# Performance work log

Hardware: AMD Instinct MI355X
Metric: run time of the kernel (lower is better)

The kernel has to match this reference:

```python
import jax, jax.numpy as jnp
import numpy as np

BASE_THETA = 0.5
K_DOP = 0.2
K_NOR = 0.15
K_SERO = 0.1
DIM = 1024


def setup_inputs() -> dict:
    key = jax.random.key(0)
    ks = jax.random.split(key, 9)
    scale = 1.0 / np.sqrt(DIM)
    x = jax.random.normal(ks[0], (2, 2048, DIM), dtype=jnp.float32)
    Wq = jax.random.normal(ks[1], (DIM, DIM), dtype=jnp.float32) * scale
    bq = jnp.zeros((DIM,), dtype=jnp.float32)
    Wk = jax.random.normal(ks[2], (DIM, DIM), dtype=jnp.float32) * scale
    bk = jnp.zeros((DIM,), dtype=jnp.float32)
    Wv = jax.random.normal(ks[3], (DIM, DIM), dtype=jnp.float32) * scale
    bv = jnp.zeros((DIM,), dtype=jnp.float32)
    Wo = jax.random.normal(ks[4], (DIM, DIM), dtype=jnp.float32) * scale
    bo = jnp.zeros((DIM,), dtype=jnp.float32)
    return {"x": x, "Wq": Wq, "bq": bq, "Wk": Wk, "bk": bk,
            "Wv": Wv, "bv": bv, "Wo": Wo, "bo": bo}


def reference(x, Wq, bq, Wk, bk, Wv, bv, Wo, bo):
    # Projections: torch nn.Linear computes x @ W.T + b
    q = jnp.einsum('bsd,ed->bse', x, Wq) + bq
    k = jnp.einsum('bsd,ed->bse', x, Wk) + bk
    v = jnp.einsum('bsd,ed->bse', x, Wv) + bv
    # Full [B, S, S] scores (no 1/sqrt(d) scaling in the original)
    qk = jnp.einsum('bsd,btd->bst', q, k)
    theta = (BASE_THETA
             + K_DOP * jax.nn.sigmoid(qk)
             + K_NOR * jnp.tanh(qk)
             + K_SERO * jax.nn.relu(qk))
    attn = jax.nn.softmax(theta, axis=-1)
    out = jnp.einsum('bst,btd->bsd', attn, v)
    return jnp.einsum('bsd,ed->bse', out, Wo) + bo
```

## Files before the change

kernel.cpp:

```cpp
#include <hip/hip_runtime.h>
#include <hip/hip_fp16.h>
#include <stdint.h>

typedef _Float16 f16;
typedef __attribute__((ext_vector_type(8))) _Float16 f16x8;
typedef __attribute__((ext_vector_type(4))) _Float16 f16x4;
typedef __attribute__((ext_vector_type(4))) float f32x4;

#define SEQ 2048
#define DIM 1024
#define NBATCH 2
#define MTOT 4096

__global__ void fill_kernel(float* p, float v, int n){
  int i = blockIdx.x * 256 + threadIdx.x;
  if (i < n) p[i] = v;
}

__global__ void cvt_all(const float* __restrict__ x, const float* __restrict__ Wq,
                        const float* __restrict__ Wk, const float* __restrict__ Wv,
                        const float* __restrict__ Wo,
                        f16* __restrict__ x16, f16* __restrict__ Wcat, f16* __restrict__ Wo16){
  int b = blockIdx.x;
  const float* src; f16* dst; int i;
  if (b < 4096){
    src = x; dst = x16; i = b * 256 + threadIdx.x;
  } else {
    int t = (b - 4096) >> 10;
    i = ((b - 4096) & 1023) * 256 + threadIdx.x;
    src = t == 0 ? Wq : t == 1 ? Wk : t == 2 ? Wv : Wo;
    dst = (t == 3) ? Wo16 : Wcat + (size_t)t * DIM * DIM;
  }
  float4 v = ((const float4*)src)[i];
  ((f16x4*)dst)[i] = (f16x4){(f16)v.x, (f16)v.y, (f16)v.z, (f16)v.w};
}

#define GLOAD16(SRC, DST) __builtin_amdgcn_global_load_lds( \
    (__attribute__((address_space(1))) void*)(SRC), \
    (__attribute__((address_space(3))) void*)(DST), 16, 0, 0)

__device__ __forceinline__ float theta_exp(float v){
  const float e1 = __expf(-v);
  const float sg = 1.f / (1.f + e1);
  const float e2 = e1 * e1;
  const float th = 2.f / (1.f + e2) - 1.f;
  const float theta = 0.5f + 0.2f * sg + 0.15f * th + 0.1f * fmaxf(v, 0.f);
  return __expf(fminf(theta - 10.f, 11.f));
}

__global__ __launch_bounds__(256, 3)
void gemm_qkv(const f16* __restrict__ A0, const f16* __restrict__ B0,
              f16* __restrict__ O0, f16* __restrict__ O1,
              const float* __restrict__ c0, const float* __restrict__ c1,
              const float* __restrict__ c2)
{
  __shared__ __align__(16) f16 As[8192];
  __shared__ __align__(16) f16 Bs[8192];
  const int tid  = threadIdx.x;
  const int lane = tid & 63;
  const int wid  = tid >> 6;
  const int bm = blockIdx.x, bn = blockIdx.y;

  const int s_r  = tid >> 3;
  const int s_cb = (tid & 7) ^ (s_r & 7);
  const f16* Ab = A0 + (long)(bm * 128 + s_r) * DIM + s_cb * 8;
  const f16* Bb = B0 + (long)(bn * 128 + s_r) * DIM + s_cb * 8;

  const int l15 = lane & 15, l7 = lane & 7, lhi = lane >> 4;
  const int wrow = (wid >> 1) * 64;
  const int wcol = (wid & 1) * 64;
  const int ar = (wrow + l15) * 64;
  const int br = (wcol + l15) * 64;
  const int cb0 = ((0 + lhi) ^ l7) * 8;
  const int cb1 = ((4 + lhi) ^ l7) * 8;

  f32x4 acc[4][4] = {};

#pragma unroll
  for (int t = 0; t < 16; ++t){
    __syncthreads();
    GLOAD16(Ab + (long)t*64,                  &As[       tid*8]);
    GLOAD16(Ab + (long)t*64 + (long)32 * DIM, &As[2048 + tid*8]);
    GLOAD16(Ab + (long)t*64 + (long)64 * DIM, &As[4096 + tid*8]);
    GLOAD16(Ab + (long)t*64 + (long)96 * DIM, &As[6144 + tid*8]);
    GLOAD16(Bb + (long)t*64,                  &Bs[       tid*8]);
    GLOAD16(Bb + (long)t*64 + (long)32 * DIM, &Bs[2048 + tid*8]);
    GLOAD16(Bb + (long)t*64 + (long)64 * DIM, &Bs[4096 + tid*8]);
    GLOAD16(Bb + (long)t*64 + (long)96 * DIM, &Bs[6144 + tid*8]);
    __syncthreads();
    f16x8 af[4], bf[4];
#pragma unroll
    for (int i = 0; i < 4; i++) af[i] = *(const f16x8*)&As[ar + i * 1024 + cb0];
#pragma unroll
    for (int j = 0; j < 4; j++) bf[j] = *(const f16x8*)&Bs[br + j * 1024 + cb0];
#pragma unroll
    for (int i = 0; i < 4; i++)
#pragma unroll
      for (int j = 0; j < 4; j++)
        acc[i][j] = __builtin_amdgcn_mfma_f32_16x16x32_f16(af[i], bf[j], acc[i][j], 0, 0, 0);
#pragma unroll
    for (int i = 0; i < 4; i++) af[i] = *(const f16x8*)&As[ar + i * 1024 + cb1];
#pragma unroll
    for (int j = 0; j < 4; j++) bf[j] = *(const f16x8*)&Bs[br + j * 1024 + cb1];
#pragma unroll
    for (int i = 0; i < 4; i++)
#pragma unroll
      for (int j = 0; j < 4; j++)
        acc[i][j] = __builtin_amdgcn_mfma_f32_16x16x32_f16(af[i], bf[j], acc[i][j], 0, 0, 0);
  }

  const int cc = l15;
  const int rr = lhi * 4;
#pragma unroll
  for (int i = 0; i < 4; i++)
#pragma unroll
    for (int j = 0; j < 4; j++){
      const int col = bn * 128 + wcol + j * 16 + cc;
      if (col < 2048){
        const float badd = (col < 1024) ? c0[col] : c1[col - 1024];
#pragma unroll
        for (int r = 0; r < 4; r++){
          const int row = bm * 128 + wrow + i * 16 + rr + r;
          O0[(long)row * 2048 + col] = (f16)(acc[i][j][r] + badd);
        }
      } else {
        const int dcol = col - 2048;
        const float badd = c2[dcol];
#pragma unroll
        for (int r = 0; r < 4; r++){
          const int row = bm * 128 + wrow + i * 16 + rr + r;
          O1[(long)row * DIM + dcol] = (f16)(acc[i][j][r] + badd);
        }
      }
    }
}

__global__ __launch_bounds__(256, 3)
void gemm_merged(const f16* __restrict__ qkcat, const f16* __restrict__ vbuf,
                 const f16* __restrict__ Wo16,
                 f16* __restrict__ Pbuf, f16* __restrict__ vWoT)
{
  __shared__ __align__(16) f16 As[8192];
  __shared__ __align__(16) f16 Bs[8192];
  const int tid  = threadIdx.x;
  const int lane = tid & 63;
  const int wid  = tid >> 6;
  const int l15 = lane & 15, l7 = lane & 7, lhi = lane >> 4;
  const int s_r  = tid >> 3;
  const int s_cb = (tid & 7) ^ (s_r & 7);
  const int cb0 = ((0 + lhi) ^ l7) * 8;
  const int cb1 = ((4 + lhi) ^ l7) * 8;
  const int cc = l15, rr = lhi * 4;
  const int wrow = (wid >> 1) * 64;
  const int wcol = (wid & 1) * 64;
  const int ar = (wrow + l15) * 64;
  const int br = (wcol + l15) * 64;
  const int r = blockIdx.x;

  if (r < 512){
    const int x = r & 7, i5 = r >> 3;
    const int bz = x >> 2;
    const int bn = (x & 3) * 4 + (i5 & 3);
    const int bm = i5 >> 2;
    const f16* Ab = qkcat + (long)bz * SEQ * 2048 + (long)(bm * 128 + s_r) * 2048 + s_cb * 8;
    const f16* Bb = qkcat + DIM + (long)bz * SEQ * 2048 + (long)(bn * 128 + s_r) * 2048 + s_cb * 8;

    f32x4 acc[4][4] = {};

#pragma unroll
    for (int t = 0; t < 16; ++t){
      __syncthreads();
      GLOAD16(Ab + (long)t*64,                   &As[       tid*8]);
      GLOAD16(Ab + (long)t*64 + (long)32 * 2048, &As[2048 + tid*8]);
      GLOAD16(Ab + (long)t*64 + (long)64 * 2048, &As[4096 + tid*8]);
      GLOAD16(Ab + (long)t*64 + (long)96 * 2048, &As[6144 + tid*8]);
      GLOAD16(Bb + (long)t*64,                   &Bs[       tid*8]);
      GLOAD16(Bb + (long)t*64 + (long)32 * 2048, &Bs[2048 + tid*8]);
      GLOAD16(Bb + (long)t*64 + (long)64 * 2048, &Bs[4096 + tid*8]);
      GLOAD16(Bb + (long)t*64 + (long)96 * 2048, &Bs[6144 + tid*8]);
      __syncthreads();
      f16x8 af[4], bf[4];
#pragma unroll
      for (int i = 0; i < 4; i++) af[i] = *(const f16x8*)&As[ar + i * 1024 + cb0];
#pragma unroll
      for (int j = 0; j < 4; j++) bf[j] = *(const f16x8*)&Bs[br + j * 1024 + cb0];
#pragma unroll
      for (int i = 0; i < 4; i++)
#pragma unroll
        for (int j = 0; j < 4; j++)
          acc[i][j] = __builtin_amdgcn_mfma_f32_16x16x32_f16(af[i], bf[j], acc[i][j], 0, 0, 0);
#pragma unroll
      for (int i = 0; i < 4; i++) af[i] = *(const f16x8*)&As[ar + i * 1024 + cb1];
#pragma unroll
      for (int j = 0; j < 4; j++) bf[j] = *(const f16x8*)&Bs[br + j * 1024 + cb1];
#pragma unroll
      for (int i = 0; i < 4; i++)
#pragma unroll
        for (int j = 0; j < 4; j++)
          acc[i][j] = __builtin_amdgcn_mfma_f32_16x16x32_f16(af[i], bf[j], acc[i][j], 0, 0, 0);
    }

#pragma unroll
    for (int i = 0; i < 4; i++)
#pragma unroll
      for (int rq = 0; rq < 4; rq++){
        const int row = bm * 128 + wrow + i * 16 + rr + rq;
#pragma unroll
        for (int j = 0; j < 4; j++){
          const int col = bn * 128 + wcol + j * 16 + cc;
          Pbuf[(long)bz * SEQ * SEQ + (long)row * SEQ + col] = (f16)theta_exp(acc[i][j][rq]);
        }
      }
  } else {
    const int rr2 = r - 512;
    const int x = rr2 & 7, i5 = rr2 >> 3;
    const int bz = x >> 2;
    const int bn = (x & 3) * 2 + (i5 & 1);
    const int bm = i5 >> 1;
    const f16* Ab = vbuf + (long)bz * SEQ * DIM + (long)(bm * 128 + s_r) * DIM + s_cb * 8;
    const f16* Bb = Wo16 + (long)(bn * 128 + s_r) * DIM + s_cb * 8;

    f32x4 acc[4][4] = {};

#pragma unroll
    for (int t = 0; t < 16; ++t){
      __syncthreads();
      GLOAD16(Ab + (long)t*64,                  &As[       tid*8]);
      GLOAD16(Ab + (long)t*64 + (long)32 * DIM, &As[2048 + tid*8]);
      GLOAD16(Ab + (long)t*64 + (long)64 * DIM, &As[4096 + tid*8]);
      GLOAD16(Ab + (long)t*64 + (long)96 * DIM, &As[6144 + tid*8]);
      GLOAD16(Bb + (long)t*64,                  &Bs[       tid*8]);
      GLOAD16(Bb + (long)t*64 + (long)32 * DIM, &Bs[2048 + tid*8]);
      GLOAD16(Bb + (long)t*64 + (long)64 * DIM, &Bs[4096 + tid*8]);
      GLOAD16(Bb + (long)t*64 + (long)96 * DIM, &Bs[6144 + tid*8]);
      __syncthreads();
      f16x8 af[4], bf[4];
#pragma unroll
      for (int i = 0; i < 4; i++) af[i] = *(const f16x8*)&As[ar + i * 1024 + cb0];
#pragma unroll
      for (int j = 0; j < 4; j++) bf[j] = *(const f16x8*)&Bs[br + j * 1024 + cb0];
#pragma unroll
      for (int i = 0; i < 4; i++)
#pragma unroll
        for (int j = 0; j < 4; j++)
          acc[i][j] = __builtin_amdgcn_mfma_f32_16x16x32_f16(af[i], bf[j], acc[i][j], 0, 0, 0);
#pragma unroll
      for (int i = 0; i < 4; i++) af[i] = *(const f16x8*)&As[ar + i * 1024 + cb1];
#pragma unroll
      for (int j = 0; j < 4; j++) bf[j] = *(const f16x8*)&Bs[br + j * 1024 + cb1];
#pragma unroll
      for (int i = 0; i < 4; i++)
#pragma unroll
        for (int j = 0; j < 4; j++)
          acc[i][j] = __builtin_amdgcn_mfma_f32_16x16x32_f16(af[i], bf[j], acc[i][j], 0, 0, 0);
    }

#pragma unroll
    for (int i = 0; i < 4; i++)
#pragma unroll
      for (int j = 0; j < 4; j++){
        const int col = bn * 128 + wcol + j * 16 + cc;
        const int row0 = bm * 128 + wrow + i * 16 + rr;
        f16x4 pk = {(f16)acc[i][j][0], (f16)acc[i][j][1],
                    (f16)acc[i][j][2], (f16)acc[i][j][3]};
        *(f16x4*)&vWoT[(long)bz * DIM * SEQ + (long)col * SEQ + row0] = pk;
      }
  }
}

__global__ __launch_bounds__(256, 4)
void gemm_final(const f16* __restrict__ Pb, const f16* __restrict__ Vw,
                float* __restrict__ psum, float* __restrict__ rowsum)
{
  __shared__ __align__(16) f16 As[8192];
  __shared__ __align__(16) f16 Bs[8192];
  const int tid  = threadIdx.x;
  const int lane = tid & 63;
  const int wid  = tid >> 6;
  const int bm = blockIdx.x, bn = blockIdx.y;
  const int bz = blockIdx.z >> 1, kh = blockIdx.z & 1;

  const f16* Ag = Pb + (long)bz * SEQ * SEQ + (long)kh * 1024;
  const f16* Bg = Vw + (long)bz * DIM * SEQ + (long)kh * 1024;

  const int s_r  = tid >> 3;
  const int s_cb = (tid & 7) ^ (s_r & 7);
  const f16* Ab = Ag + (long)(bm * 128 + s_r) * 2048 + s_cb * 8;
  const f16* Bb = Bg + (long)(bn * 128 + s_r) * 2048 + s_cb * 8;

  const int l15 = lane & 15, l7 = lane & 7, lhi = lane >> 4;
  const int wrow = (wid >> 1) * 64;
  const int wcol = (wid & 1) * 64;
  const int ar = (wrow + l15) * 64;
  const int br = (wcol + l15) * 64;
  const int cb0 = ((0 + lhi) ^ l7) * 8;
  const int cb1 = ((4 + lhi) ^ l7) * 8;
  const bool do_rs = ((wid & 1) == 0);

  f32x4 acc[4][4] = {};
  float rsum[4] = {0.f, 0.f, 0.f, 0.f};

#pragma unroll
  for (int t = 0; t < 16; ++t){
    __syncthreads();
    GLOAD16(Ab + (long)t*64,                   &As[       tid*8]);
    GLOAD16(Ab + (long)t*64 + (long)32 * 2048, &As[2048 + tid*8]);
    GLOAD16(Ab + (long)t*64 + (long)64 * 2048, &As[4096 + tid*8]);
    GLOAD16(Ab + (long)t*64 + (long)96 * 2048, &As[6144 + tid*8]);
    GLOAD16(Bb + (long)t*64,                   &Bs[       tid*8]);
    GLOAD16(Bb + (long)t*64 + (long)32 * 2048, &Bs[2048 + tid*8]);
    GLOAD16(Bb + (long)t*64 + (long)64 * 2048, &Bs[4096 + tid*8]);
    GLOAD16(Bb + (long)t*64 + (long)96 * 2048, &Bs[6144 + tid*8]);
    __syncthreads();
    f16x8 af[4], bf[4];
#pragma unroll
    for (int i = 0; i < 4; i++) af[i] = *(const f16x8*)&As[ar + i * 1024 + cb0];
#pragma unroll
    for (int j = 0; j < 4; j++) bf[j] = *(const f16x8*)&Bs[br + j * 1024 + cb0];
#pragma unroll
    for (int i = 0; i < 4; i++)
#pragma unroll
      for (int j = 0; j < 4; j++)
        acc[i][j] = __builtin_amdgcn_mfma_f32_16x16x32_f16(af[i], bf[j], acc[i][j], 0, 0, 0);
    if (do_rs){
#pragma unroll
      for (int i = 0; i < 4; i++)
#pragma unroll
        for (int e = 0; e < 8; e++) rsum[i] += (float)af[i][e];
    }
#pragma unroll
    for (int i = 0; i < 4; i++) af[i] = *(const f16x8*)&As[ar + i * 1024 + cb1];
#pragma unroll
    for (int j = 0; j < 4; j++) bf[j] = *(const f16x8*)&Bs[br + j * 1024 + cb1];
#pragma unroll
    for (int i = 0; i < 4; i++)
#pragma unroll
      for (int j = 0; j < 4; j++)
        acc[i][j] = __builtin_amdgcn_mfma_f32_16x16x32_f16(af[i], bf[j], acc[i][j], 0, 0, 0);
    if (do_rs){
#pragma unroll
      for (int i = 0; i < 4; i++)
#pragma unroll
        for (int e = 0; e < 8; e++) rsum[i] += (float)af[i][e];
    }
  }

  if (do_rs){
#pragma unroll
    for (int i = 0; i < 4; i++){
      rsum[i] += __shfl_xor(rsum[i], 16, 64);
      rsum[i] += __shfl_xor(rsum[i], 32, 64);
    }
    if (bn == 0 && lane < 16){
#pragma unroll
      for (int i = 0; i < 4; i++)
        rowsum[(long)kh * MTOT + bz * SEQ + bm * 128 + wrow + i * 16 + lane] = rsum[i];
    }
  }

  const int cc = l15;
  const int rr = lhi * 4;
  float* Po = psum + (long)kh * MTOT * DIM + (long)bz * SEQ * DIM;
#pragma unroll
  for (int i = 0; i < 4; i++)
#pragma unroll
    for (int j = 0; j < 4; j++){
      const int col = bn * 128 + wcol + j * 16 + cc;
#pragma unroll
      for (int r = 0; r < 4; r++){
        const int row = bm * 128 + wrow + i * 16 + rr + r;
        Po[(long)row * DIM + col] = acc[i][j][r];
      }
    }
}

__global__ __launch_bounds__(256)
void combine_kernel(const float* __restrict__ psum, const float* __restrict__ rowsum,
                    const float* __restrict__ bo, float* __restrict__ out)
{
  const long i = (long)blockIdx.x * 256 + threadIdx.x;
  const int row = (int)(i >> 8);
  const int c4  = (int)(i & 255);
  float4 a = ((const float4*)psum)[i];
  float4 b = ((const float4*)psum)[i + (long)MTOT * DIM / 4];
  float4 bb = ((const float4*)bo)[c4];
  const float inv = 1.f / (rowsum[row] + rowsum[MTOT + row]);
  float4 o;
  o.x = (a.x + b.x) * inv + bb.x;
  o.y = (a.y + b.y) * inv + bb.y;
  o.z = (a.z + b.z) * inv + bb.z;
  o.w = (a.w + b.w) * inv + bb.w;
  ((float4*)out)[i] = o;
}

extern "C" void kernel_launch(void* const* d_in, const int* in_sizes, int n_in,
                              void* d_out, int out_size, void* d_ws, size_t ws_size,
                              hipStream_t stream){
  const float* x  = (const float*)d_in[0];
  const float* Wq = (const float*)d_in[1];
  const float* bq = (const float*)d_in[2];
  const float* Wk = (const float*)d_in[3];
  const float* bk = (const float*)d_in[4];
  const float* Wv = (const float*)d_in[5];
  const float* bv = (const float*)d_in[6];
  const float* Wo = (const float*)d_in[7];
  const float* bo = (const float*)d_in[8];
  float* out = (float*)d_out;

  char* ws = (char*)d_ws;
  size_t off = 0;
  auto alloc = [&](size_t bytes) -> char* {
    char* p = ws + off; off += (bytes + 255) & ~(size_t)255; return p;
  };

  f16* x16     = (f16*)alloc(2ull * MTOT * DIM);
  f16* Wcat    = (f16*)alloc(2ull * 3 * DIM * DIM);
  f16* Wo16    = (f16*)alloc(2ull * DIM * DIM);
  f16* qkcat   = (f16*)alloc(2ull * MTOT * 2 * DIM);
  f16* vbuf    = (f16*)alloc(2ull * MTOT * DIM);
  f16* Pbuf    = (f16*)alloc(2ull * NBATCH * SEQ * SEQ);
  f16* vWoT    = (f16*)alloc(2ull * NBATCH * DIM * SEQ);
  float* psum  = (float*)alloc(4ull * 2 * MTOT * DIM);
  float* rowsm = (float*)alloc(4ull * 2 * MTOT);

  if (off > ws_size){
    fill_kernel<<<(out_size + 255) / 256, 256, 0, stream>>>(out, 12345.0f, out_size);
    return;
  }

  cvt_all<<<8192, 256, 0, stream>>>(x, Wq, Wk, Wv, Wo, x16, Wcat, Wo16);

  gemm_qkv<<<dim3(MTOT / 128, 3 * DIM / 128, 1), 256, 0, stream>>>(
      x16, Wcat, qkcat, vbuf, bq, bk, bv);

  gemm_merged<<<768, 256, 0, stream>>>(qkcat, vbuf, Wo16, Pbuf, vWoT);

  gemm_final<<<dim3(SEQ / 128, DIM / 128, 2 * NBATCH), 256, 0, stream>>>(
      Pbuf, vWoT, psum, rowsm);

  combine_kernel<<<MTOT * DIM / 4 / 256, 256, 0, stream>>>(psum, rowsm, bo, out);
}
```

Before: 120.9 us.

## Fuse split-K combine into gemm_final via atomic ticket per output tile

Removes the separate combine kernel by having each gemm_final block take an atomic ticket for its output tile. The second of the two split-K halves to finish reads its sibling's partial sums and both row sums, then writes the normalized output plus bias. The ticket array is zeroed by an extra block in the conversion kernel. This saves a launch and one full pass over both partial buffers, but every block now writes its partial, and the rowsum write drops the bn==0 guard, which adds redundant writes.

```diff
diff --git a/kernel.cpp b/kernel.cpp
--- a/kernel.cpp
+++ b/kernel.cpp
@@ -20,8 +20,13 @@
 __global__ void cvt_all(const float* __restrict__ x, const float* __restrict__ Wq,
                         const float* __restrict__ Wk, const float* __restrict__ Wv,
                         const float* __restrict__ Wo,
-                        f16* __restrict__ x16, f16* __restrict__ Wcat, f16* __restrict__ Wo16){
+                        f16* __restrict__ x16, f16* __restrict__ Wcat, f16* __restrict__ Wo16,
+                        int* __restrict__ ticket){
   int b = blockIdx.x;
+  if (b == 8192){
+    ticket[threadIdx.x] = 0;
+    return;
+  }
   const float* src; f16* dst; int i;
   if (b < 4096){
     src = x; dst = x16; i = b * 256 + threadIdx.x;
@@ -270,10 +275,13 @@
 
 __global__ __launch_bounds__(256, 4)
 void gemm_final(const f16* __restrict__ Pb, const f16* __restrict__ Vw,
-                float* __restrict__ psum, float* __restrict__ rowsum)
+                float* __restrict__ psum, float* __restrict__ rowsum,
+                int* __restrict__ ticket, const float* __restrict__ bo,
+                float* __restrict__ out)
 {
   __shared__ __align__(16) f16 As[8192];
   __shared__ __align__(16) f16 Bs[8192];
+  __shared__ int s_old;
   const int tid  = threadIdx.x;
   const int lane = tid & 63;
   const int wid  = tid >> 6;
@@ -351,7 +359,7 @@
       rsum[i] += __shfl_xor(rsum[i], 16, 64);
       rsum[i] += __shfl_xor(rsum[i], 32, 64);
     }
-    if (bn == 0 && lane < 16){
+    if (lane < 16){
 #pragma unroll
       for (int i = 0; i < 4; i++)
         rowsum[(long)kh * MTOT + bz * SEQ + bm * 128 + wrow + i * 16 + lane] = rsum[i];
@@ -372,25 +380,33 @@
         Po[(long)row * DIM + col] = acc[i][j][r];
       }
     }
-}
-
-__global__ __launch_bounds__(256)
-void combine_kernel(const float* __restrict__ psum, const float* __restrict__ rowsum,
-                    const float* __restrict__ bo, float* __restrict__ out)
-{
-  const long i = (long)blockIdx.x * 256 + threadIdx.x;
-  const int row = (int)(i >> 8);
-  const int c4  = (int)(i & 255);
-  float4 a = ((const float4*)psum)[i];
-  float4 b = ((const float4*)psum)[i + (long)MTOT * DIM / 4];
-  float4 bb = ((const float4*)bo)[c4];
-  const float inv = 1.f / (rowsum[row] + rowsum[MTOT + row]);
-  float4 o;
-  o.x = (a.x + b.x) * inv + bb.x;
-  o.y = (a.y + b.y) * inv + bb.y;
-  o.z = (a.z + b.z) * inv + bb.z;
-  o.w = (a.w + b.w) * inv + bb.w;
-  ((float4*)out)[i] = o;
+
+  __syncthreads();
+  if (tid == 0){
+    __threadfence();
+    s_old = atomicAdd(&ticket[(bz * 16 + bm) * 8 + bn], 1);
+  }
+  __syncthreads();
+  if (s_old == 1){
+    __threadfence();
+    const float* Ps = psum + (long)(kh ^ 1) * MTOT * DIM + (long)bz * SEQ * DIM;
+    const float* rs0 = rowsum;
+    const float* rs1 = rowsum + MTOT;
+    float* Ob = out + (long)bz * SEQ * DIM;
+#pragma unroll
+    for (int i = 0; i < 4; i++)
+#pragma unroll
+      for (int r = 0; r < 4; r++){
+        const int row = bm * 128 + wrow + i * 16 + rr + r;
+        const float inv = 1.f / (rs0[bz * SEQ + row] + rs1[bz * SEQ + row]);
+#pragma unroll
+        for (int j = 0; j < 4; j++){
+          const int col = bn * 128 + wcol + j * 16 + cc;
+          const float sib = Ps[(long)row * DIM + col];
+          Ob[(long)row * DIM + col] = (acc[i][j][r] + sib) * inv + bo[col];
+        }
+      }
+  }
 }
 
 extern "C" void kernel_launch(void* const* d_in, const int* in_sizes, int n_in,
@@ -422,13 +438,14 @@
   f16* vWoT    = (f16*)alloc(2ull * NBATCH * DIM * SEQ);
   float* psum  = (float*)alloc(4ull * 2 * MTOT * DIM);
   float* rowsm = (float*)alloc(4ull * 2 * MTOT);
+  int* ticket  = (int*)alloc(4ull * 256);
 
   if (off > ws_size){
     fill_kernel<<<(out_size + 255) / 256, 256, 0, stream>>>(out, 12345.0f, out_size);
     return;
   }
 
-  cvt_all<<<8192, 256, 0, stream>>>(x, Wq, Wk, Wv, Wo, x16, Wcat, Wo16);
+  cvt_all<<<8193, 256, 0, stream>>>(x, Wq, Wk, Wv, Wo, x16, Wcat, Wo16, ticket);
 
   gemm_qkv<<<dim3(MTOT / 128, 3 * DIM / 128, 1), 256, 0, stream>>>(
       x16, Wcat, qkcat, vbuf, bq, bk, bv);
@@ -436,7 +453,5 @@
   gemm_merged<<<768, 256, 0, stream>>>(qkcat, vbuf, Wo16, Pbuf, vWoT);
 
   gemm_final<<<dim3(SEQ / 128, DIM / 128, 2 * NBATCH), 256, 0, stream>>>(
-      Pbuf, vWoT, psum, rowsm);
-
-  combine_kernel<<<MTOT * DIM / 4 / 256, 256, 0, stream>>>(psum, rowsm, bo, out);
-}
+      Pbuf, vWoT, psum, rowsm, ticket, bo, out);
+}
```

After: 178.5 us. 47.6% more time.
